# Optimization experiments

Measured on AMD Instinct MI355X. Metric: run time of the kernel, lower is better.

The kernel has to match this reference:

```python
import jax, jax.numpy as jnp
import numpy as np

SCALE = 0.125  # 1/sqrt(d_k), d_k = 64


def setup_inputs() -> dict:
    key = jax.random.key(0)
    kq, kk, kv, kp = jax.random.split(key, 4)
    H, B, L, T, D = 16, 4, 1024, 1024, 64
    return {
        "query": jax.random.normal(kq, (H, B, L, D), dtype=jnp.float32),
        "key": jax.random.normal(kk, (H, B, T, D), dtype=jnp.float32),
        "value": jax.random.normal(kv, (H, B, T, D), dtype=jnp.float32),
        "prev_attention": jax.random.normal(kp, (H, B, L, T), dtype=jnp.float32),
    }


def reference(query, key, value, prev_attention):
    # scores: [h, b, l, t]
    scores = jnp.einsum("hblk,hbtk->hblt", query, key) * SCALE
    scores = scores + prev_attention
    attention = jax.nn.softmax(scores, axis=-1)
    # dropout disabled (rate 0.0) for deterministic reference
    output = jnp.einsum("hblt,hbtv->hblv", attention, value)
    return (output, attention)
```

## Files before the change

kernel.cpp:

```cpp
#include <hip/hip_runtime.h>

#define SCALE 0.125f

constexpr int L_ = 1024, T_ = 1024, D_ = 64, HB_ = 64;

using f32x4 = __attribute__((ext_vector_type(4))) float;
using half8 = __attribute__((ext_vector_type(8))) _Float16;
using half4 = __attribute__((ext_vector_type(4))) _Float16;

__global__ __launch_bounds__(256) void cvt_v(const float* __restrict__ v,
                                             _Float16* __restrict__ vh) {
  __shared__ _Float16 ts[64][136];
  const int tid = threadIdx.x;
  const int hb = blockIdx.y;
  const int t0 = blockIdx.x * 128;
  {
    const int tr = tid >> 1, dh = (tid & 1) * 32;
    const float* p = v + ((size_t)hb * T_ + t0 + tr) * D_ + dh;
#pragma unroll
    for (int i = 0; i < 8; ++i) {
      f32x4 r = *(const f32x4*)(p + i * 4);
#pragma unroll
      for (int e = 0; e < 4; ++e) ts[dh + i * 4 + e][tr] = (_Float16)r[e];
    }
  }
  __syncthreads();
  {
    const int d = tid >> 2, tq = (tid & 3) * 32;
    _Float16* qo = vh + ((size_t)hb * D_ + d) * T_ + t0 + tq;
#pragma unroll
    for (int i = 0; i < 4; ++i)
      *(half8*)(qo + i * 8) = *(const half8*)&ts[d][tq + i * 8];
  }
}

__global__ __launch_bounds__(512) void attn_all(
    const float* __restrict__ q, const float* __restrict__ kk,
    const _Float16* __restrict__ Vh, const float* __restrict__ prev,
    float* __restrict__ out, float* __restrict__ att) {
  __shared__ __align__(16) _Float16 Ks[1024][70];
  __shared__ __align__(16) _Float16 El[8][16][72];

  const int ltile = blockIdx.x;
  const int hb    = blockIdx.y;
  const int tid = threadIdx.x;
  const int w = tid >> 6, l = tid & 63, l15 = l & 15, lg = l >> 4;
  const int qrow = ltile * 128 + w * 16 + l15;

  {
    const int srow = tid >> 2, scol = (tid & 3) * 16;
    const float* kp0 = kk + (size_t)hb * T_ * D_;
#pragma unroll
    for (int rep = 0; rep < 8; ++rep) {
      const int r = rep * 128 + srow;
      const float* p = kp0 + (size_t)r * D_ + scol;
      f32x4 a = *(const f32x4*)(p);
      f32x4 b = *(const f32x4*)(p + 4);
      f32x4 cc = *(const f32x4*)(p + 8);
      f32x4 d = *(const f32x4*)(p + 12);
      half8 h0, h1;
#pragma unroll
      for (int e = 0; e < 4; ++e) {
        h0[e] = (_Float16)a[e];  h0[4 + e] = (_Float16)b[e];
        h1[e] = (_Float16)cc[e]; h1[4 + e] = (_Float16)d[e];
      }
      *(half8*)&Ks[r][scol] = h0;
      *(half8*)&Ks[r][scol + 8] = h1;
    }
  }

  half8 qb2[2];
  {
    const float* qp = q + ((size_t)hb * L_ + qrow) * D_ + lg * 8;
#pragma unroll
    for (int f = 0; f < 2; ++f)
#pragma unroll
      for (int e = 0; e < 8; ++e) qb2[f][e] = (_Float16)qp[f * 32 + e];
  }

  const float* prow = prev + ((size_t)hb * L_ + qrow) * (size_t)T_;

  f32x4 pb[2][4];
  auto pload = [&](int c, int s) {
#pragma unroll
    for (int nt = 0; nt < 4; ++nt)
      pb[s][nt] = *(const f32x4*)(prow + c * 64 + nt * 16 + lg * 4);
  };

  __syncthreads();

  pload(0, 0);
  pload(1, 1);
  float zsum = 0.f;

#pragma unroll 2
  for (int c = 0; c < 16; ++c) {
    f32x4 pvv[4];
#pragma unroll
    for (int nt = 0; nt < 4; ++nt) pvv[nt] = pb[c & 1][nt];
    if (c < 14) pload(c + 2, c & 1);

#pragma unroll
    for (int nt = 0; nt < 4; ++nt) {
      const int trow = c * 64 + nt * 16 + l15;
      half8 ka0 = *(const half8*)&Ks[trow][lg * 8];
      half8 ka1 = *(const half8*)&Ks[trow][32 + lg * 8];
      f32x4 acc = {0.f, 0.f, 0.f, 0.f};
      acc = __builtin_amdgcn_mfma_f32_16x16x32_f16(ka0, qb2[0], acc, 0, 0, 0);
      acc = __builtin_amdgcn_mfma_f32_16x16x32_f16(ka1, qb2[1], acc, 0, 0, 0);
      zsum += __expf(acc[0] * SCALE + pvv[nt][0]);
      zsum += __expf(acc[1] * SCALE + pvv[nt][1]);
      zsum += __expf(acc[2] * SCALE + pvv[nt][2]);
      zsum += __expf(acc[3] * SCALE + pvv[nt][3]);
    }
  }

  zsum += __shfl_xor(zsum, 16, 64);
  zsum += __shfl_xor(zsum, 32, 64);
  const float rzq = 1.0f / zsum;

  const _Float16* vbh = Vh + (size_t)hb * D_ * T_;
  float* arow = att + ((size_t)hb * L_ + qrow) * (size_t)T_;

  pload(0, 0);
  pload(1, 1);

  f32x4 oacc[4];
#pragma unroll
  for (int nd = 0; nd < 4; ++nd) oacc[nd] = (f32x4){0.f, 0.f, 0.f, 0.f};

#pragma unroll 2
  for (int c = 0; c < 16; ++c) {
    half8 vr[8];
#pragma unroll
    for (int ks = 0; ks < 2; ++ks)
#pragma unroll
      for (int nd = 0; nd < 4; ++nd)
        vr[ks * 4 + nd] = *(const half8*)(vbh + (size_t)(nd * 16 + l15) * T_ +
                                          c * 64 + ks * 32 + lg * 8);

    f32x4 pvv[4];
#pragma unroll
    for (int nt = 0; nt < 4; ++nt) pvv[nt] = pb[c & 1][nt];
    if (c < 14) pload(c + 2, c & 1);

#pragma unroll
    for (int nt = 0; nt < 4; ++nt) {
      const int trow = c * 64 + nt * 16 + l15;
      half8 ka0 = *(const half8*)&Ks[trow][lg * 8];
      half8 ka1 = *(const half8*)&Ks[trow][32 + lg * 8];
      f32x4 acc = {0.f, 0.f, 0.f, 0.f};
      acc = __builtin_amdgcn_mfma_f32_16x16x32_f16(ka0, qb2[0], acc, 0, 0, 0);
      acc = __builtin_amdgcn_mfma_f32_16x16x32_f16(ka1, qb2[1], acc, 0, 0, 0);

      f32x4 s;
      s[0] = __expf(acc[0] * SCALE + pvv[nt][0]) * rzq;
      s[1] = __expf(acc[1] * SCALE + pvv[nt][1]) * rzq;
      s[2] = __expf(acc[2] * SCALE + pvv[nt][2]) * rzq;
      s[3] = __expf(acc[3] * SCALE + pvv[nt][3]) * rzq;
      *(f32x4*)(arow + c * 64 + nt * 16 + lg * 4) = s;

      half4 ev;
      ev[0] = (_Float16)s[0]; ev[1] = (_Float16)s[1];
      ev[2] = (_Float16)s[2]; ev[3] = (_Float16)s[3];
      *(half4*)&El[w][l15][nt * 16 + lg * 4] = ev;
    }

#pragma unroll
    for (int ks = 0; ks < 2; ++ks) {
      half8 af = *(const half8*)&El[w][l15][ks * 32 + lg * 8];
#pragma unroll
      for (int nd = 0; nd < 4; ++nd)
        oacc[nd] = __builtin_amdgcn_mfma_f32_16x16x32_f16(af, vr[ks * 4 + nd],
                                                          oacc[nd], 0, 0, 0);
    }
  }

  float* outw =
      out + ((size_t)hb * L_ + ltile * 128 + w * 16 + lg * 4) * (size_t)D_;
#pragma unroll
  for (int nd = 0; nd < 4; ++nd)
#pragma unroll
    for (int i = 0; i < 4; ++i)
      outw[(size_t)i * D_ + nd * 16 + l15] = oacc[nd][i];
}

extern "C" void kernel_launch(void* const* d_in, const int* in_sizes, int n_in,
                              void* d_out, int out_size, void* d_ws,
                              size_t ws_size, hipStream_t stream) {
  const float* q    = (const float*)d_in[0];
  const float* k    = (const float*)d_in[1];
  const float* v    = (const float*)d_in[2];
  const float* prev = (const float*)d_in[3];

  float* out = (float*)d_out;
  float* att = out + (size_t)HB_ * L_ * D_;

  _Float16* Vh = (_Float16*)d_ws;

  cvt_v<<<dim3(T_ / 128, HB_), 256, 0, stream>>>(v, Vh);
  attn_all<<<dim3(L_ / 128, HB_), 512, 0, stream>>>(q, k, Vh, prev, out, att);
}
```

Before: 228.0 us.

## Use 1024-thread blocks and feed P·V MFMA from registers instead of LDS

Doubles the query rows per block to 256 with 1024 threads. This halves how often each block stages K into LDS and fits the grid in a single wave of one block per CU. It also removes the per-wave El LDS buffer: the softmax probabilities go straight into the MFMA A operand as half8 values whose upper four lanes are zero, with V loaded as half4 to match. The cost is twice as many P·V MFMAs doing half-useful work and higher register pressure per thread at 1024 threads.

```diff
diff --git a/kernel.cpp b/kernel.cpp
--- a/kernel.cpp
+++ b/kernel.cpp
@@ -34,25 +34,24 @@
   }
 }
 
-__global__ __launch_bounds__(512) void attn_all(
+__global__ __launch_bounds__(1024) void attn_all(
     const float* __restrict__ q, const float* __restrict__ kk,
     const _Float16* __restrict__ Vh, const float* __restrict__ prev,
     float* __restrict__ out, float* __restrict__ att) {
   __shared__ __align__(16) _Float16 Ks[1024][70];
-  __shared__ __align__(16) _Float16 El[8][16][72];
 
   const int ltile = blockIdx.x;
   const int hb    = blockIdx.y;
   const int tid = threadIdx.x;
   const int w = tid >> 6, l = tid & 63, l15 = l & 15, lg = l >> 4;
-  const int qrow = ltile * 128 + w * 16 + l15;
+  const int qrow = ltile * 256 + w * 16 + l15;
 
   {
     const int srow = tid >> 2, scol = (tid & 3) * 16;
     const float* kp0 = kk + (size_t)hb * T_ * D_;
 #pragma unroll
-    for (int rep = 0; rep < 8; ++rep) {
-      const int r = rep * 128 + srow;
+    for (int rep = 0; rep < 4; ++rep) {
+      const int r = rep * 256 + srow;
       const float* p = kp0 + (size_t)r * D_ + scol;
       f32x4 a = *(const f32x4*)(p);
       f32x4 b = *(const f32x4*)(p + 4);
@@ -131,13 +130,13 @@
 
 #pragma unroll 2
   for (int c = 0; c < 16; ++c) {
-    half8 vr[8];
-#pragma unroll
-    for (int ks = 0; ks < 2; ++ks)
+    half4 vr[4][4];
+#pragma unroll
+    for (int nt = 0; nt < 4; ++nt)
 #pragma unroll
       for (int nd = 0; nd < 4; ++nd)
-        vr[ks * 4 + nd] = *(const half8*)(vbh + (size_t)(nd * 16 + l15) * T_ +
-                                          c * 64 + ks * 32 + lg * 8);
+        vr[nt][nd] = *(const half4*)(vbh + (size_t)(nd * 16 + l15) * T_ +
+                                     c * 64 + nt * 16 + lg * 4);
 
     f32x4 pvv[4];
 #pragma unroll
@@ -160,24 +159,24 @@
       s[3] = __expf(acc[3] * SCALE + pvv[nt][3]) * rzq;
       *(f32x4*)(arow + c * 64 + nt * 16 + lg * 4) = s;
 
-      half4 ev;
-      ev[0] = (_Float16)s[0]; ev[1] = (_Float16)s[1];
-      ev[2] = (_Float16)s[2]; ev[3] = (_Float16)s[3];
-      *(half4*)&El[w][l15][nt * 16 + lg * 4] = ev;
-    }
-
-#pragma unroll
-    for (int ks = 0; ks < 2; ++ks) {
-      half8 af = *(const half8*)&El[w][l15][ks * 32 + lg * 8];
-#pragma unroll
-      for (int nd = 0; nd < 4; ++nd)
-        oacc[nd] = __builtin_amdgcn_mfma_f32_16x16x32_f16(af, vr[ks * 4 + nd],
-                                                          oacc[nd], 0, 0, 0);
+      half8 af;
+      af[0] = (_Float16)s[0]; af[1] = (_Float16)s[1];
+      af[2] = (_Float16)s[2]; af[3] = (_Float16)s[3];
+      af[4] = af[5] = af[6] = af[7] = (_Float16)0.f;
+#pragma unroll
+      for (int nd = 0; nd < 4; ++nd) {
+        half8 vb;
+        vb[0] = vr[nt][nd][0]; vb[1] = vr[nt][nd][1];
+        vb[2] = vr[nt][nd][2]; vb[3] = vr[nt][nd][3];
+        vb[4] = vb[5] = vb[6] = vb[7] = (_Float16)0.f;
+        oacc[nd] =
+            __builtin_amdgcn_mfma_f32_16x16x32_f16(af, vb, oacc[nd], 0, 0, 0);
+      }
     }
   }
 
   float* outw =
-      out + ((size_t)hb * L_ + ltile * 128 + w * 16 + lg * 4) * (size_t)D_;
+      out + ((size_t)hb * L_ + ltile * 256 + w * 16 + lg * 4) * (size_t)D_;
 #pragma unroll
   for (int nd = 0; nd < 4; ++nd)
 #pragma unroll
@@ -199,5 +198,5 @@
   _Float16* Vh = (_Float16*)d_ws;
 
   cvt_v<<<dim3(T_ / 128, HB_), 256, 0, stream>>>(v, Vh);
-  attn_all<<<dim3(L_ / 128, HB_), 512, 0, stream>>>(q, k, Vh, prev, out, att);
+  attn_all<<<dim3(L_ / 256, HB_), 1024, 0, stream>>>(q, k, Vh, prev, out, att);
 }
```

Result: slower. 323.8 us (+42.0%).
